# Performance work log

Hardware: AMD Instinct MI355X
Metric: run time of the kernel (lower is better)

## Reference

```python
import jax, jax.numpy as jnp
import numpy as np

D, N, L, H, VOCAB = 256, 8192, 6, 4, 256
EPS = 1e-5


def layernorm(x):
    # LayerNorm over last dim, no affine (matches nn.LayerNorm(D, elementwise_affine=False))
    mu = jnp.mean(x, axis=-1, keepdims=True)
    var = jnp.mean(jnp.square(x - mu), axis=-1, keepdims=True)
    return (x - mu) * jax.lax.rsqrt(var + EPS)


def rotate_half(x):
    x1, x2 = jnp.split(x, 2, axis=-1)
    return jnp.concatenate((-x2, x1), axis=-1)


def rope_tables(T, dim, dtype):
    inv_freq = 1.0 / (10000.0 ** (jnp.arange(0, dim, 2, dtype=jnp.float32) / dim))
    t = jnp.arange(T, dtype=jnp.float32)
    freqs = jnp.einsum('i,j->ij', t, inv_freq)          # [T, dim/2]
    emb = jnp.concatenate((freqs, freqs), axis=-1)       # [T, dim]
    return jnp.cos(emb).astype(dtype), jnp.sin(emb).astype(dtype)


def linear_attention(Q, K, V):
    # unnormalized causal attention with RoPE on Q, K
    B, T, d = Q.shape
    cos, sin = rope_tables(T, d, Q.dtype)
    Qr = Q * cos + rotate_half(Q) * sin
    Kr = K * cos + rotate_half(K) * sin
    energy = jnp.einsum('btd,bsd->bts', Qr, Kr)          # [B, T, T]
    mask = jnp.tril(jnp.ones((T, T), dtype=energy.dtype))
    energy = energy * mask
    return jnp.einsum('bts,bsd->btd', energy, V)


def setup_inputs() -> dict:
    key = jax.random.key(0)
    ks = jax.random.split(key, 6)
    idx = jax.random.randint(ks[0], (4, 2048), 0, VOCAB)
    wte = jax.random.normal(ks[1], (VOCAB, D), dtype=jnp.float32) * 0.02
    encoder = jax.random.normal(ks[2], (N, D), dtype=jnp.float32) * 0.02
    decoder_x = jax.random.normal(ks[3], (H, D, N // H), dtype=jnp.float32) * 0.02
    decoder_y = jax.random.normal(ks[4], (H, D, N // H), dtype=jnp.float32) * 0.02
    readout = jax.random.normal(ks[5], (D, VOCAB), dtype=jnp.float32) * 0.02
    return {"idx": idx, "wte": wte, "encoder": encoder,
            "decoder_x": decoder_x, "decoder_y": decoder_y, "readout": readout}


def reference(idx, wte, encoder, decoder_x, decoder_y, readout):
    B, T = idx.shape
    v_ast = layernorm(wte[idx])                          # [B, T, D]
    for _ in range(L):
        x_raw = jnp.einsum('btd,hdm->bthm', v_ast, decoder_x)
        x = jax.nn.relu(x_raw)                           # [B, T, H, N/H]
        a_ast = linear_attention(v_ast, v_ast, v_ast)
        y_raw = jnp.einsum('btd,hdm->bthm', layernorm(a_ast), decoder_y)
        y = jax.nn.relu(y_raw) * x
        y_flat = y.reshape(B, T, -1)                     # [B, T, N]
        update = y_flat @ encoder                        # [B, T, D]
        v_ast = v_ast + layernorm(update)
    logits = v_ast @ readout                             # [B, T, VOCAB]
    return logits
```

## Files before the change

### kernel.cpp

```cpp
#include <hip/hip_runtime.h>
#include <hip/hip_bf16.h>

typedef __hip_bfloat16 bf16;
typedef _Float16 half_t;
typedef __attribute__((ext_vector_type(8))) _Float16 half8;
typedef __attribute__((ext_vector_type(4))) float f32x4;

#define LN_EPS 1e-5f

static constexpr int Dk     = 256;
static constexpr int Tk     = 2048;
static constexpr int BTk    = 8192;
static constexpr int MHk    = 2048;
static constexpr int Nk     = 8192;
static constexpr int LAYERS = 6;
static constexpr long long TD  = (long long)Tk * Dk;
static constexpr long long BTD = (long long)BTk * Dk;
static constexpr long long TT  = (long long)Tk * Tk;

#define PA_SCALE 0.00390625f

#define SKQ(t) ((((t) & 3) ^ (((t) >> 3) & 3)) * 8)

__device__ __forceinline__ float wave_reduce(float v) {
#pragma unroll
    for (int o = 32; o > 0; o >>= 1) v += __shfl_down(v, o);
    return v;
}

__device__ __forceinline__ float block_sum_256(float x, float* sbuf) {
    float s = wave_reduce(x);
    int lane = threadIdx.x & 63, wv = threadIdx.x >> 6;
    if (lane == 0) sbuf[wv] = s;
    __syncthreads();
    float r = sbuf[0] + sbuf[1] + sbuf[2] + sbuf[3];
    __syncthreads();
    return r;
}

__device__ __forceinline__ void glds16(const void* g, void* lds) {
    __builtin_amdgcn_global_load_lds(
        (const __attribute__((address_space(1))) void*)g,
        (__attribute__((address_space(3))) void*)lds, 16, 0, 0);
}

__device__ __forceinline__ void rope_row(const float* nv, int t, half_t* qrow) {
    int i = threadIdx.x;
    if (i < 128) {
        float invf = powf(10000.f, -(float)i / 128.f);
        float ang = (float)t * invf;
        float s, c;
        sincosf(ang, &s, &c);
        float q1 = nv[i], q2 = nv[128 + i];
        qrow[i]       = (half_t)(q1 * c - q2 * s);
        qrow[128 + i] = (half_t)(q2 * c + q1 * s);
    }
}

__global__ __launch_bounds__(256) void sniff_kernel(const unsigned short* __restrict__ w,
                                                    int* __restrict__ flag) {
    __shared__ float sbuf[4];
    int tid = threadIdx.x;
    float cnt = 0.f;
    for (int i = tid; i < 1024; i += 256) {
        int e = (w[i] >> 7) & 0xFF;
        if (e >= 128) cnt += 1.f;
    }
    float tot = block_sum_256(cnt, sbuf);
    if (tid == 0) *flag = (tot > 32.f) ? 1 : 0;
}

__global__ __launch_bounds__(256) void tr_cvt16_kernel(const void* __restrict__ src,
                                                       const int* __restrict__ flag,
                                                       half_t* __restrict__ dst,
                                                       int R, int C,
                                                       long long sz, long long dz) {
    __shared__ float t[32][33];
    bool f32 = (*flag != 0);
    int ct = blockIdx.x * 32, rt = blockIdx.y * 32;
    long long so = (long long)blockIdx.z * sz, dofs = (long long)blockIdx.z * dz;
    int tx = threadIdx.x & 31, ty = threadIdx.x >> 5;
#pragma unroll
    for (int i = 0; i < 4; i++) {
        long long idx = so + (long long)(rt + ty + i * 8) * C + ct + tx;
        t[ty + i * 8][tx] = f32 ? ((const float*)src)[idx] : (float)((const bf16*)src)[idx];
    }
    __syncthreads();
#pragma unroll
    for (int i = 0; i < 4; i++) {
        long long odx = dofs + (long long)(ct + ty + i * 8) * R + rt + tx;
        dst[odx] = (half_t)t[tx][ty + i * 8];
    }
}

__global__ __launch_bounds__(256) void trv_kernel(const float* __restrict__ src,
                                                  half_t* __restrict__ dst) {
    __shared__ float t[32][33];
    int ct = blockIdx.x * 32, rt = blockIdx.y * 32;
    int tx = threadIdx.x & 31, ty = threadIdx.x >> 5;
#pragma unroll
    for (int i = 0; i < 4; i++)
        t[ty + i * 8][tx] = src[(long long)(rt + ty + i * 8) * Dk + ct + tx];
    __syncthreads();
#pragma unroll
    for (int i = 0; i < 4; i++)
        dst[(long long)(ct + ty + i * 8) * BTk + rt + tx] = (half_t)t[tx][ty + i * 8];
}

__global__ __launch_bounds__(256) void embed_ln_kernel(const int* __restrict__ idx,
                                                       const void* __restrict__ wte,
                                                       const int* __restrict__ flag,
                                                       float* __restrict__ v,
                                                       half_t* __restrict__ vf,
                                                       half_t* __restrict__ qf) {
    __shared__ float sbuf[4];
    __shared__ float nvs[256];
    int bt = blockIdx.x, tid = threadIdx.x;
    int id = idx[bt];
    bool f32 = (*flag != 0);
    float x = f32 ? ((const float*)wte)[id * Dk + tid]
                  : (float)((const bf16*)wte)[id * Dk + tid];
    float mu = block_sum_256(x, sbuf) * (1.f / 256.f);
    float d = x - mu;
    float var = block_sum_256(d * d, sbuf) * (1.f / 256.f);
    float r = d * rsqrtf(var + LN_EPS);
    v[bt * Dk + tid] = r;
    vf[bt * Dk + tid] = (half_t)r;
    nvs[tid] = r;
    __syncthreads();
    rope_row(nvs, bt & (Tk - 1), qf + (long long)bt * Dk);
}

__global__ __launch_bounds__(256) void ln_rows_kernel(const half_t* __restrict__ Pa,
                                                      half_t* __restrict__ of) {
    __shared__ float sbuf[4];
    int bt = blockIdx.x, tid = threadIdx.x;
    int b = bt >> 11, t = bt & (Tk - 1);
    int ncnt = ((t & ~127) >> 9) + 1;
    const half_t* p = Pa + ((long long)(b << 2)) * TD + (long long)t * Dk + tid;
    float x = 0.f;
    for (int c = 0; c < ncnt; c++) x += (float)p[(long long)c * TD];
    float mu = block_sum_256(x, sbuf) * (1.f / 256.f);
    float d = x - mu;
    float var = block_sum_256(d * d, sbuf) * (1.f / 256.f);
    float r = d * rsqrtf(var + LN_EPS);
    of[bt * Dk + tid] = (half_t)r;
}

__global__ __launch_bounds__(256) void add_ln_kernel(const half_t* __restrict__ Pu,
                                                     float* __restrict__ v,
                                                     half_t* __restrict__ vf,
                                                     half_t* __restrict__ qf) {
    __shared__ float sbuf[4];
    __shared__ float nvs[256];
    int bt = blockIdx.x, tid = threadIdx.x;
    long long e = (long long)bt * Dk + tid;
    float x = (float)Pu[e] + (float)Pu[e + BTD]
            + (float)Pu[e + 2 * BTD] + (float)Pu[e + 3 * BTD];
    float mu = block_sum_256(x, sbuf) * (1.f / 256.f);
    float d = x - mu;
    float var = block_sum_256(d * d, sbuf) * (1.f / 256.f);
    float r = d * rsqrtf(var + LN_EPS);
    float nv = v[e] + r;
    v[e] = nv;
    vf[e] = (half_t)nv;
    nvs[tid] = nv;
    __syncthreads();
    rope_row(nvs, bt & (Tk - 1), qf + (long long)bt * Dk);
}

__global__ __launch_bounds__(256) void gemm128e(
    const half_t* __restrict__ Q, half_t* __restrict__ E) {
    __shared__ __align__(16) half_t As[128 * 32];
    __shared__ __align__(16) half_t Bs[128 * 32];
    const int tid = threadIdx.x;
    const int lane = tid & 63, wv = tid >> 6;
    const int wr = wv >> 1, wc = wv & 1;
    const int quad = lane >> 4, r = lane & 15;
    const int qsw = (quad ^ ((r >> 1) & 3)) * 8;
    const int mb = blockIdx.y * 128, nb = blockIdx.x * 128;
    if ((int)blockIdx.x > (int)blockIdx.y) return;
    const half_t* Qb = Q + (long long)blockIdx.z * TD;
    half_t* Eb = E + (long long)blockIdx.z * TT;

    f32x4 acc[4][4] = {};
    const int srow = tid >> 2, skq = SKQ(tid);
    const int wbase = (tid & 192) * 8;
    for (int k0 = 0; k0 < Dk; k0 += 32) {
#pragma unroll
        for (int rnd = 0; rnd < 2; rnd++) {
            int row = rnd * 64 + srow;
            glds16(Qb + (long long)(mb + row) * Dk + k0 + skq, As + rnd * 2048 + wbase);
            glds16(Qb + (long long)(nb + row) * Dk + k0 + skq, Bs + rnd * 2048 + wbase);
        }
        __syncthreads();
        half8 bfr[4];
#pragma unroll
        for (int ni = 0; ni < 4; ni++)
            bfr[ni] = *(const half8*)&Bs[(wc * 64 + ni * 16 + r) * 32 + qsw];
#pragma unroll
        for (int mi = 0; mi < 4; mi++) {
            half8 afr = *(const half8*)&As[(wr * 64 + mi * 16 + r) * 32 + qsw];
#pragma unroll
            for (int ni = 0; ni < 4; ni++)
                acc[mi][ni] = __builtin_amdgcn_mfma_f32_16x16x32_f16(afr, bfr[ni], acc[mi][ni], 0, 0, 0);
        }
        __syncthreads();
    }
#pragma unroll
    for (int mi = 0; mi < 4; mi++)
#pragma unroll
        for (int ni = 0; ni < 4; ni++) {
            int row0 = mb + wr * 64 + mi * 16 + quad * 4;
            int col = nb + wc * 64 + ni * 16 + r;
#pragma unroll
            for (int rr = 0; rr < 4; rr++) {
                int row = row0 + rr;
                float val = (row < col) ? 0.f : acc[mi][ni][rr];
                Eb[(long long)row * Tk + col] = (half_t)val;
            }
        }
}

__global__ __launch_bounds__(256) void gemm128a(
    const half_t* __restrict__ E, const half_t* __restrict__ vT,
    half_t* __restrict__ Pa) {
    __shared__ __align__(16) half_t As[128 * 32];
    __shared__ __align__(16) half_t Bs[128 * 32];
    const int tid = threadIdx.x;
    const int lane = tid & 63, wv = tid >> 6;
    const int wr = wv >> 1, wc = wv & 1;
    const int quad = lane >> 4, r = lane & 15;
    const int qsw = (quad ^ ((r >> 1) & 3)) * 8;
    const int mb = blockIdx.x * 128, nb = blockIdx.y * 128;
    const int b = blockIdx.z >> 2, c = blockIdx.z & 3;
    const int kbeg = c * 512;
    const int kend = min(mb + 128, kbeg + 512);
    if (kend <= kbeg) return;

    const half_t* Ab = E + (long long)b * TT;
    const half_t* Bb = vT + (long long)b * Tk;
    half_t* Pc = Pa + (long long)blockIdx.z * TD;
    f32x4 acc[4][4] = {};
    const int srow = tid >> 2, skq = SKQ(tid);
    const int wbase = (tid & 192) * 8;
    for (int k0 = kbeg; k0 < kend; k0 += 32) {
#pragma unroll
        for (int rnd = 0; rnd < 2; rnd++) {
            int row = rnd * 64 + srow;
            glds16(Ab + (long long)(mb + row) * Tk + k0 + skq, As + rnd * 2048 + wbase);
            glds16(Bb + (long long)(nb + row) * BTk + k0 + skq, Bs + rnd * 2048 + wbase);
        }
        __syncthreads();
        half8 bfr[4];
#pragma unroll
        for (int ni = 0; ni < 4; ni++)
            bfr[ni] = *(const half8*)&Bs[(wc * 64 + ni * 16 + r) * 32 + qsw];
#pragma unroll
        for (int mi = 0; mi < 4; mi++) {
            half8 afr = *(const half8*)&As[(wr * 64 + mi * 16 + r) * 32 + qsw];
#pragma unroll
            for (int ni = 0; ni < 4; ni++)
                acc[mi][ni] = __builtin_amdgcn_mfma_f32_16x16x32_f16(afr, bfr[ni], acc[mi][ni], 0, 0, 0);
        }
        __syncthreads();
    }
#pragma unroll
    for (int mi = 0; mi < 4; mi++)
#pragma unroll
        for (int ni = 0; ni < 4; ni++) {
            int row0 = mb + wr * 64 + mi * 16 + quad * 4;
            int col = nb + wc * 64 + ni * 16 + r;
#pragma unroll
            for (int rr = 0; rr < 4; rr++)
                Pc[(long long)(row0 + rr) * Dk + col] = (half_t)(acc[mi][ni][rr] * PA_SCALE);
        }
}

__global__ __launch_bounds__(256, 2) void dual_gemm(
    const half_t* __restrict__ A1,
    const half_t* __restrict__ A2,
    const half_t* __restrict__ dxT,
    const half_t* __restrict__ dyT,
    half_t* __restrict__ C) {
    __shared__ __align__(16) half_t As1[128 * 64];
    __shared__ __align__(16) half_t As2[128 * 64];
    __shared__ __align__(16) half_t Bs1[128 * 64];
    __shared__ __align__(16) half_t Bs2[128 * 64];
    const int tid = threadIdx.x;
    const int lane = tid & 63, wv = tid >> 6;
    const int wr = wv >> 1, wc = wv & 1;
    const int quad = lane >> 4, r = lane & 15;
    const int flat = blockIdx.x + 16 * (blockIdx.y + 64 * blockIdx.z);
    const int xcd = flat & 7, j = flat >> 3;
    const int mt = (xcd >> 2) * 32 + (j >> 4);
    const int nt = (xcd & 3) * 4 + (j & 3);
    const int h  = (j >> 2) & 3;
    const int mb = mt * 128, nb = nt * 128;
    const half_t* B1 = dxT + (long long)h * MHk * Dk;
    const half_t* B2 = dyT + (long long)h * MHk * Dk;

    f32x4 accX[4][4] = {};
    f32x4 accY[4][4] = {};
    const int srow8 = lane >> 3;
    const int soct  = (lane & 7) ^ srow8;
    for (int k0 = 0; k0 < Dk; k0 += 64) {
#pragma unroll
        for (int c = 0; c < 4; c++) {
            int row = wv * 32 + c * 8;
            long long ga = (long long)(mb + row + srow8) * Dk + k0 + soct * 8;
            long long gb = (long long)(nb + row + srow8) * Dk + k0 + soct * 8;
            glds16(A1 + ga, As1 + row * 64);
            glds16(A2 + ga, As2 + row * 64);
            glds16(B1 + gb, Bs1 + row * 64);
            glds16(B2 + gb, Bs2 + row * 64);
        }
        __syncthreads();
#pragma unroll
        for (int sub = 0; sub < 2; sub++) {
            half8 b1f[4], b2f[4];
#pragma unroll
            for (int ni = 0; ni < 4; ni++) {
                int R = wc * 64 + ni * 16 + r;
                int pos = ((sub * 4 + quad) ^ (R & 7)) * 8;
                b1f[ni] = *(const half8*)&Bs1[R * 64 + pos];
                b2f[ni] = *(const half8*)&Bs2[R * 64 + pos];
            }
#pragma unroll
            for (int mi = 0; mi < 4; mi++) {
                int R = wr * 64 + mi * 16 + r;
                int pos = ((sub * 4 + quad) ^ (R & 7)) * 8;
                half8 a1 = *(const half8*)&As1[R * 64 + pos];
                half8 a2 = *(const half8*)&As2[R * 64 + pos];
#pragma unroll
                for (int ni = 0; ni < 4; ni++) {
                    accX[mi][ni] = __builtin_amdgcn_mfma_f32_16x16x32_f16(a1, b1f[ni], accX[mi][ni], 0, 0, 0);
                    accY[mi][ni] = __builtin_amdgcn_mfma_f32_16x16x32_f16(a2, b2f[ni], accY[mi][ni], 0, 0, 0);
                }
            }
        }
        __syncthreads();
    }
#pragma unroll
    for (int mi = 0; mi < 4; mi++)
#pragma unroll
        for (int ni = 0; ni < 4; ni++) {
            int row0 = mb + wr * 64 + mi * 16 + quad * 4;
            int col = h * MHk + nb + wc * 64 + ni * 16 + r;
#pragma unroll
            for (int rr = 0; rr < 4; rr++) {
                float val = fmaxf(accY[mi][ni][rr], 0.f) * fmaxf(accX[mi][ni][rr], 0.f);
                C[(long long)(row0 + rr) * Nk + col] = (half_t)val;
            }
        }
}

__global__ __launch_bounds__(256, 2) void gemm128u(
    const half_t* __restrict__ A, const half_t* __restrict__ B,
    half_t* __restrict__ Pu) {
    __shared__ __align__(16) half_t As[4][128 * 32];
    __shared__ __align__(16) half_t Bs[4][128 * 32];
    const int tid = threadIdx.x;
    const int lane = tid & 63, wv = tid >> 6;
    const int wr = wv >> 1, wc = wv & 1;
    const int quad = lane >> 4, r = lane & 15;
    const int qsw = (quad ^ ((r >> 1) & 3)) * 8;
    const int flat = blockIdx.x;
    const int xcd = flat & 7, j = flat >> 3;
    const int nb = (j & 1) * 128;
    const int kc = (j >> 1) & 3;
    const int mb = (xcd * 8 + (j >> 3)) * 128;
    const int kbeg = kc * 2048;
    half_t* Pc = Pu + (long long)kc * BTD;

    f32x4 acc[4][4] = {};
    const int srow = tid >> 2, skq = SKQ(tid);
    const int wbase = (tid & 192) * 8;

    auto stage = [&](int ks) {
        const int k0 = kbeg + ks * 32;
        const int bsel = ks & 3;
#pragma unroll
        for (int rnd = 0; rnd < 2; rnd++) {
            int row = rnd * 64 + srow;
            glds16(A + (long long)(mb + row) * Nk + k0 + skq, &As[bsel][rnd * 2048 + wbase]);
            glds16(B + (long long)(nb + row) * Nk + k0 + skq, &Bs[bsel][rnd * 2048 + wbase]);
        }
    };
    auto compute = [&](int ks) {
        const int cur = ks & 3;
        half8 bfr[4];
#pragma unroll
        for (int ni = 0; ni < 4; ni++)
            bfr[ni] = *(const half8*)&Bs[cur][(wc * 64 + ni * 16 + r) * 32 + qsw];
#pragma unroll
        for (int mi = 0; mi < 4; mi++) {
            half8 afr = *(const half8*)&As[cur][(wr * 64 + mi * 16 + r) * 32 + qsw];
#pragma unroll
            for (int ni = 0; ni < 4; ni++)
                acc[mi][ni] = __builtin_amdgcn_mfma_f32_16x16x32_f16(afr, bfr[ni], acc[mi][ni], 0, 0, 0);
        }
    };

    stage(0); stage(1); stage(2);
    for (int ks = 0; ks < 61; ks++) {
        asm volatile("s_waitcnt vmcnt(8)" ::: "memory");
        __builtin_amdgcn_s_barrier();
        __builtin_amdgcn_sched_barrier(0);
        stage(ks + 3);
        __builtin_amdgcn_s_setprio(1);
        compute(ks);
        __builtin_amdgcn_s_setprio(0);
    }
    asm volatile("s_waitcnt vmcnt(8)" ::: "memory");
    __builtin_amdgcn_s_barrier();
    __builtin_amdgcn_sched_barrier(0);
    compute(61);
    asm volatile("s_waitcnt vmcnt(4)" ::: "memory");
    __builtin_amdgcn_s_barrier();
    __builtin_amdgcn_sched_barrier(0);
    compute(62);
    asm volatile("s_waitcnt vmcnt(0)" ::: "memory");
    __builtin_amdgcn_s_barrier();
    __builtin_amdgcn_sched_barrier(0);
    compute(63);

#pragma unroll
    for (int mi = 0; mi < 4; mi++)
#pragma unroll
        for (int ni = 0; ni < 4; ni++) {
            int row0 = mb + wr * 64 + mi * 16 + quad * 4;
            int col = nb + wc * 64 + ni * 16 + r;
#pragma unroll
            for (int rr = 0; rr < 4; rr++)
                Pc[(long long)(row0 + rr) * Dk + col] = (half_t)acc[mi][ni][rr];
        }
}

__global__ __launch_bounds__(256) void gemm64h(
    const half_t* __restrict__ A, int lda,
    const half_t* __restrict__ B, int ldb,
    float* __restrict__ C, int ldc, int K) {
    __shared__ __align__(16) half_t As[64 * 32];
    __shared__ __align__(16) half_t Bs[64 * 32];
    const int tid = threadIdx.x;
    const int lane = tid & 63, wv = tid >> 6;
    const int wr = wv >> 1, wc = wv & 1;
    const int quad = lane >> 4, r = lane & 15;
    const int qsw = (quad ^ ((r >> 1) & 3)) * 8;
    const int mb = blockIdx.y * 64, nb = blockIdx.x * 64;

    f32x4 acc[2][2] = {};
    const int srow = tid >> 2, skq = SKQ(tid);
    const int wbase = (tid & 192) * 8;
    for (int k0 = 0; k0 < K; k0 += 32) {
        glds16(A + (long long)(mb + srow) * lda + k0 + skq, As + wbase);
        glds16(B + (long long)(nb + srow) * ldb + k0 + skq, Bs + wbase);
        __syncthreads();
        half8 b0 = *(const half8*)&Bs[(wc * 32 +  0 + r) * 32 + qsw];
        half8 b1 = *(const half8*)&Bs[(wc * 32 + 16 + r) * 32 + qsw];
#pragma unroll
        for (int mi = 0; mi < 2; mi++) {
            half8 afr = *(const half8*)&As[(wr * 32 + mi * 16 + r) * 32 + qsw];
            acc[mi][0] = __builtin_amdgcn_mfma_f32_16x16x32_f16(afr, b0, acc[mi][0], 0, 0, 0);
            acc[mi][1] = __builtin_amdgcn_mfma_f32_16x16x32_f16(afr, b1, acc[mi][1], 0, 0, 0);
        }
        __syncthreads();
    }
#pragma unroll
    for (int mi = 0; mi < 2; mi++)
#pragma unroll
        for (int ni = 0; ni < 2; ni++) {
            int row0 = mb + wr * 32 + mi * 16 + quad * 4;
            int col = nb + wc * 32 + ni * 16 + r;
#pragma unroll
            for (int rr = 0; rr < 4; rr++)
                C[(long long)(row0 + rr) * ldc + col] = acc[mi][ni][rr];
        }
}

extern "C" void kernel_launch(void* const* d_in, const int* in_sizes, int n_in,
                              void* d_out, int out_size, void* d_ws, size_t ws_size,
                              hipStream_t stream) {
    (void)in_sizes; (void)n_in; (void)out_size; (void)ws_size;
    const int* idx = (const int*)d_in[0];
    float* out = (float*)d_out;

    char* ws = (char*)d_ws;
    float*  v32  = (float*) (ws);
    half_t* vf   = (half_t*)(ws + (  8ll << 20));
    half_t* qf   = (half_t*)(ws + ( 12ll << 20));
    half_t* vT   = (half_t*)(ws + ( 16ll << 20));
    half_t* lnf  = (half_t*)(ws + ( 20ll << 20));
    half_t* E    = (half_t*)(ws + ( 24ll << 20));
    half_t* Pa   = (half_t*)(ws + ( 56ll << 20));
    half_t* Pu   = (half_t*)(ws + ( 24ll << 20));
    half_t* y16  = (half_t*)(ws + ( 88ll << 20));
    half_t* dxT  = (half_t*)(ws + (216ll << 20));
    half_t* dyT  = (half_t*)(ws + (220ll << 20));
    half_t* eT   = (half_t*)(ws + (224ll << 20));
    half_t* roT  = (half_t*)(ws + (228ll << 20));
    int*    flag = (int*)   (ws + (228ll << 20) + (256ll << 10));

    sniff_kernel<<<1, 256, 0, stream>>>((const unsigned short*)d_in[1], flag);
    tr_cvt16_kernel<<<dim3(MHk / 32, Dk / 32, 4), 256, 0, stream>>>(
        d_in[3], flag, dxT, Dk, MHk, (long long)Dk * MHk, (long long)Dk * MHk);
    tr_cvt16_kernel<<<dim3(MHk / 32, Dk / 32, 4), 256, 0, stream>>>(
        d_in[4], flag, dyT, Dk, MHk, (long long)Dk * MHk, (long long)Dk * MHk);
    tr_cvt16_kernel<<<dim3(Dk / 32, Nk / 32, 1), 256, 0, stream>>>(
        d_in[2], flag, eT, Nk, Dk, 0, 0);
    tr_cvt16_kernel<<<dim3(Dk / 32, Dk / 32, 1), 256, 0, stream>>>(
        d_in[5], flag, roT, Dk, Dk, 0, 0);

    embed_ln_kernel<<<BTk, 256, 0, stream>>>(idx, d_in[1], flag, v32, vf, qf);

    for (int l = 0; l < LAYERS; l++) {
        trv_kernel<<<dim3(Dk / 32, BTk / 32), 256, 0, stream>>>(v32, vT);
        gemm128e<<<dim3(Tk / 128, Tk / 128, 4), 256, 0, stream>>>(qf, E);
        gemm128a<<<dim3(Tk / 128, Dk / 128, 16), 256, 0, stream>>>(E, vT, Pa);
        ln_rows_kernel<<<BTk, 256, 0, stream>>>(Pa, lnf);
        dual_gemm<<<dim3(MHk / 128, BTk / 128, 4), 256, 0, stream>>>(
            vf, lnf, dxT, dyT, y16);
        gemm128u<<<dim3(512), 256, 0, stream>>>(y16, eT, Pu);
        add_ln_kernel<<<BTk, 256, 0, stream>>>(Pu, v32, vf, qf);
    }
    gemm64h<<<dim3(Dk / 64, BTk / 64), 256, 0, stream>>>(
        vf, Dk, roT, Dk, out, Dk, Dk);
}
```

Measured before the change: 1.291 ms.

## Double-buffer dual_gemm LDS with k=32 stages and async prefetch pipeline

Replaces the single-buffered 64-wide K tile in dual_gemm with a two-stage ring of 32-wide K tiles. The next stage's global-to-LDS loads are issued while the current stage is computed, using explicit vmcnt waits, barriers and raised wave priority around the MFMA block. The aim is to overlap memory latency with matrix math. It also changes the LDS swizzle to the SKQ/qsw scheme. The risk lies in the hand-tuned waitcnt counts and the swizzle correctness.

```diff
diff --git a/kernel.cpp b/kernel.cpp
--- a/kernel.cpp
+++ b/kernel.cpp
@@ -283,14 +283,15 @@
     const half_t* __restrict__ dxT,
     const half_t* __restrict__ dyT,
     half_t* __restrict__ C) {
-    __shared__ __align__(16) half_t As1[128 * 64];
-    __shared__ __align__(16) half_t As2[128 * 64];
-    __shared__ __align__(16) half_t Bs1[128 * 64];
-    __shared__ __align__(16) half_t Bs2[128 * 64];
+    __shared__ __align__(16) half_t As1[2][128 * 32];
+    __shared__ __align__(16) half_t As2[2][128 * 32];
+    __shared__ __align__(16) half_t Bs1[2][128 * 32];
+    __shared__ __align__(16) half_t Bs2[2][128 * 32];
     const int tid = threadIdx.x;
     const int lane = tid & 63, wv = tid >> 6;
     const int wr = wv >> 1, wc = wv & 1;
     const int quad = lane >> 4, r = lane & 15;
+    const int qsw = (quad ^ ((r >> 1) & 3)) * 8;
     const int flat = blockIdx.x + 16 * (blockIdx.y + 64 * blockIdx.z);
     const int xcd = flat & 7, j = flat >> 3;
     const int mt = (xcd >> 2) * 32 + (j >> 4);
@@ -302,45 +303,66 @@
 
     f32x4 accX[4][4] = {};
     f32x4 accY[4][4] = {};
-    const int srow8 = lane >> 3;
-    const int soct  = (lane & 7) ^ srow8;
-    for (int k0 = 0; k0 < Dk; k0 += 64) {
-#pragma unroll
-        for (int c = 0; c < 4; c++) {
-            int row = wv * 32 + c * 8;
-            long long ga = (long long)(mb + row + srow8) * Dk + k0 + soct * 8;
-            long long gb = (long long)(nb + row + srow8) * Dk + k0 + soct * 8;
-            glds16(A1 + ga, As1 + row * 64);
-            glds16(A2 + ga, As2 + row * 64);
-            glds16(B1 + gb, Bs1 + row * 64);
-            glds16(B2 + gb, Bs2 + row * 64);
-        }
-        __syncthreads();
-#pragma unroll
-        for (int sub = 0; sub < 2; sub++) {
-            half8 b1f[4], b2f[4];
+    const int srow = tid >> 2, skq = SKQ(tid);
+    const int wbase = (tid & 192) * 8;
+
+    auto stage = [&](int ks) {
+        const int k0 = ks * 32;
+        const int bsel = ks & 1;
+#pragma unroll
+        for (int rnd = 0; rnd < 2; rnd++) {
+            int row = rnd * 64 + srow;
+            long long ga = (long long)(mb + row) * Dk + k0 + skq;
+            long long gb = (long long)(nb + row) * Dk + k0 + skq;
+            glds16(A1 + ga, &As1[bsel][rnd * 2048 + wbase]);
+            glds16(A2 + ga, &As2[bsel][rnd * 2048 + wbase]);
+            glds16(B1 + gb, &Bs1[bsel][rnd * 2048 + wbase]);
+            glds16(B2 + gb, &Bs2[bsel][rnd * 2048 + wbase]);
+        }
+    };
+    auto compute = [&](int ks) {
+        const int cur = ks & 1;
+        half8 b1f[4], b2f[4];
+#pragma unroll
+        for (int ni = 0; ni < 4; ni++) {
+            int R = wc * 64 + ni * 16 + r;
+            b1f[ni] = *(const half8*)&Bs1[cur][R * 32 + qsw];
+            b2f[ni] = *(const half8*)&Bs2[cur][R * 32 + qsw];
+        }
+#pragma unroll
+        for (int mi = 0; mi < 4; mi++) {
+            int R = wr * 64 + mi * 16 + r;
+            half8 a1 = *(const half8*)&As1[cur][R * 32 + qsw];
+            half8 a2 = *(const half8*)&As2[cur][R * 32 + qsw];
 #pragma unroll
             for (int ni = 0; ni < 4; ni++) {
-                int R = wc * 64 + ni * 16 + r;
-                int pos = ((sub * 4 + quad) ^ (R & 7)) * 8;
-                b1f[ni] = *(const half8*)&Bs1[R * 64 + pos];
-                b2f[ni] = *(const half8*)&Bs2[R * 64 + pos];
+                accX[mi][ni] = __builtin_amdgcn_mfma_f32_16x16x32_f16(a1, b1f[ni], accX[mi][ni], 0, 0, 0);
+                accY[mi][ni] = __builtin_amdgcn_mfma_f32_16x16x32_f16(a2, b2f[ni], accY[mi][ni], 0, 0, 0);
             }
-#pragma unroll
-            for (int mi = 0; mi < 4; mi++) {
-                int R = wr * 64 + mi * 16 + r;
-                int pos = ((sub * 4 + quad) ^ (R & 7)) * 8;
-                half8 a1 = *(const half8*)&As1[R * 64 + pos];
-                half8 a2 = *(const half8*)&As2[R * 64 + pos];
-#pragma unroll
-                for (int ni = 0; ni < 4; ni++) {
-                    accX[mi][ni] = __builtin_amdgcn_mfma_f32_16x16x32_f16(a1, b1f[ni], accX[mi][ni], 0, 0, 0);
-                    accY[mi][ni] = __builtin_amdgcn_mfma_f32_16x16x32_f16(a2, b2f[ni], accY[mi][ni], 0, 0, 0);
-                }
-            }
-        }
-        __syncthreads();
-    }
+        }
+    };
+
+    stage(0); stage(1);
+    for (int ks = 0; ks < 6; ks++) {
+        asm volatile("s_waitcnt vmcnt(8)" ::: "memory");
+        __builtin_amdgcn_s_barrier();
+        __builtin_amdgcn_sched_barrier(0);
+        __builtin_amdgcn_s_setprio(1);
+        compute(ks);
+        __builtin_amdgcn_s_setprio(0);
+        __builtin_amdgcn_s_barrier();
+        __builtin_amdgcn_sched_barrier(0);
+        stage(ks + 2);
+    }
+    asm volatile("s_waitcnt vmcnt(8)" ::: "memory");
+    __builtin_amdgcn_s_barrier();
+    __builtin_amdgcn_sched_barrier(0);
+    compute(6);
+    asm volatile("s_waitcnt vmcnt(0)" ::: "memory");
+    __builtin_amdgcn_s_barrier();
+    __builtin_amdgcn_sched_barrier(0);
+    compute(7);
+
 #pragma unroll
     for (int mi = 0; mi < 4; mi++)
 #pragma unroll
```

Result: slower. 1.382 ms (+7.0%).
